# Kernel tuning notes

Hardware: AMD Instinct MI355X
Metric: run time of the kernel (lower is better)

The kernel has to match this reference:

```python
import jax, jax.numpy as jnp
import numpy as np

B, C, O, H, W = 16, 256, 256, 64, 64
T_DIM, E, K = 512, 4, 3


def setup_inputs() -> dict:
    key = jax.random.key(0)
    ks = jax.random.split(key, 12)
    def rn(k, shape, s=0.02):
        return jax.random.normal(k, shape, jnp.float32) * s
    return dict(
        x=jax.random.normal(ks[0], (B, C, H, W), jnp.float32),
        time_emb=jax.random.normal(ks[1], (B, T_DIM), jnp.float32),
        Wq=rn(ks[2], (C, T_DIM)), bq=jnp.zeros((C,), jnp.float32),
        Wk=rn(ks[3], (C, C)), bk=jnp.zeros((C,), jnp.float32),
        Wv=rn(ks[4], (C, C)), bv=jnp.zeros((C,), jnp.float32),
        Wm1=rn(ks[5], (C // 4, C)), bm1=jnp.zeros((C // 4,), jnp.float32),
        Wm2=rn(ks[6], (C, C // 4)), bm2=jnp.zeros((C,), jnp.float32),
        Wc=rn(ks[7], (E, C)), bc=jnp.zeros((E,), jnp.float32),
        expert_w=rn(ks[8], (E, O, C, K, K), s=0.05),  # [E, O, C_in/groups, K, K]
        expert_b=rn(ks[9], (E, O), s=0.05),
    )


def reference(x, time_emb, Wq, bq, Wk, bk, Wv, bv, Wm1, bm1, Wm2, bm2, Wc, bc, expert_w, expert_b):
    # --- router (eval mode: no gating noise) ---
    pooled = x.mean(axis=(2, 3))                      # [B, C] == avg_pool over full HxW
    q = time_emb @ Wq.T + bq                          # [B, C]
    k = pooled @ Wk.T + bk                            # [B, C]
    attn = jax.nn.sigmoid(q * k)
    v = pooled @ Wv.T + bv
    x_att = v * attn
    h = jax.nn.gelu(x_att @ Wm1.T + bm1, approximate=False) @ Wm2.T + bm2
    x_mix = x_att + h
    logits = x_mix @ Wc.T + bc                        # [B, E]
    rw = jnp.tanh(logits)                             # routing weights [B, E]

    # --- per-sample expert-weight mixing ---
    w_eff = jnp.einsum('be,eoihw->boihw', rw, expert_w)  # [B, O, C, K, K]
    b_eff = rw @ expert_b                                 # [B, O]

    # --- per-sample conv (equivalent to groups=B trick) ---
    def conv_one(xb, wb):
        # xb: [C, H, W], wb: [O, C, K, K]
        return jax.lax.conv_general_dilated(
            xb[None], wb, window_strides=(1, 1), padding=[(1, 1), (1, 1)],
            dimension_numbers=('NCHW', 'OIHW', 'NCHW'))[0]

    out = jax.vmap(conv_one)(x, w_eff)                 # [B, O, H, W]
    return out + b_eff[:, :, None, None]
```

## Files before the change

### kernel.cpp

```cpp
#include <hip/hip_runtime.h>


typedef __bf16 bf16x8 __attribute__((ext_vector_type(8)));
typedef float f32x4 __attribute__((ext_vector_type(4)));

__device__ __forceinline__ unsigned short f2bf(float f) {
  union { float f; unsigned int u; } v;
  v.f = f;
  unsigned int r = v.u + 0x7FFFu + ((v.u >> 16) & 1u);
  return (unsigned short)(r >> 16);
}

__device__ __forceinline__ void load_lds16(const void* g, void* l) {
  __builtin_amdgcn_global_load_lds(
      (__attribute__((address_space(1))) void*)(void*)g,
      (__attribute__((address_space(3))) void*)l, 16, 0, 0);
}

__global__ void pool_kernel(const float* __restrict__ x, float* __restrict__ pooled) {
  int bc = blockIdx.x;
  const float* p = x + (size_t)bc * 4096;
  int t = threadIdx.x;
  float s = 0.f;
  for (int i = t; i < 4096; i += 256) s += p[i];
  __shared__ float red[4];
  #pragma unroll
  for (int off = 32; off > 0; off >>= 1) s += __shfl_down(s, off);
  if ((t & 63) == 0) red[t >> 6] = s;
  __syncthreads();
  if (t == 0) pooled[bc] = (red[0] + red[1] + red[2] + red[3]) * (1.0f / 4096.0f);
}

__global__ void transpose_kernel(const float* __restrict__ x, unsigned short* __restrict__ xT) {
  int bh = blockIdx.x;
  int b = bh >> 6, h = bh & 63;
  __shared__ unsigned short lds[256][68];
  int t = threadIdx.x;
  int w = t & 63, cg = t >> 6;
  for (int it = 0; it < 64; ++it) {
    int c = it * 4 + cg;
    float v = x[(((size_t)(b * 256 + c)) * 64 + h) * 64 + w];
    lds[c][w] = f2bf(v);
  }
  __syncthreads();
  size_t obase = (size_t)bh * 64 * 256;
  for (int ww = 0; ww < 64; ++ww) {
    xT[obase + (size_t)ww * 256 + t] = lds[t][ww];
  }
}

__global__ void router_kernel(
    const float* __restrict__ time_emb, const float* __restrict__ pooled,
    const float* __restrict__ Wq, const float* __restrict__ bq,
    const float* __restrict__ Wk, const float* __restrict__ bk,
    const float* __restrict__ Wv, const float* __restrict__ bv,
    const float* __restrict__ Wm1, const float* __restrict__ bm1,
    const float* __restrict__ Wm2, const float* __restrict__ bm2,
    const float* __restrict__ Wc, const float* __restrict__ bc,
    const float* __restrict__ expert_b,
    float* __restrict__ rw_out, float* __restrict__ beff_out) {
  int b = blockIdx.x, t = threadIdx.x;
  __shared__ float te[512], pl[256], xa[256], m1s[64], xms[256], rws[4];
  te[t] = time_emb[b * 512 + t];
  te[t + 256] = time_emb[b * 512 + 256 + t];
  pl[t] = pooled[b * 256 + t];
  __syncthreads();
  float q = bq[t], k = bk[t], v = bv[t];
  const float* wq = Wq + (size_t)t * 512;
  for (int i = 0; i < 512; ++i) q += te[i] * wq[i];
  const float* wk = Wk + (size_t)t * 256;
  const float* wv = Wv + (size_t)t * 256;
  for (int i = 0; i < 256; ++i) { float p = pl[i]; k += p * wk[i]; v += p * wv[i]; }
  float attn = 1.0f / (1.0f + expf(-(q * k)));
  float xatt = v * attn;
  xa[t] = xatt;
  __syncthreads();
  if (t < 64) {
    float s = bm1[t];
    const float* w1 = Wm1 + (size_t)t * 256;
    for (int i = 0; i < 256; ++i) s += xa[i] * w1[i];
    m1s[t] = 0.5f * s * (1.0f + erff(s * 0.7071067811865476f));
  }
  __syncthreads();
  float hsum = bm2[t];
  const float* w2 = Wm2 + (size_t)t * 64;
  for (int j = 0; j < 64; ++j) hsum += m1s[j] * w2[j];
  float xm = xatt + hsum;
  xms[t] = xm;
  __syncthreads();
  if (t < 4) {
    float s = bc[t];
    const float* wc = Wc + (size_t)t * 256;
    for (int i = 0; i < 256; ++i) s += xms[i] * wc[i];
    float r = tanhf(s);
    rws[t] = r;
    rw_out[b * 4 + t] = r;
  }
  __syncthreads();
  float be = 0.f;
  #pragma unroll
  for (int e = 0; e < 4; ++e) be += rws[e] * expert_b[e * 256 + t];
  beff_out[b * 256 + t] = be;
}

__global__ void wmix_kernel(const float* __restrict__ ew, const float* __restrict__ rw,
                            unsigned short* __restrict__ wmix) {
  int o = blockIdx.x & 255;
  int b0 = (blockIdx.x >> 8) << 2;
  int c = threadIdx.x;
  float wv[4][9];
  #pragma unroll
  for (int e = 0; e < 4; ++e) {
    const float* s = ew + (((size_t)e * 256 + o) * 256 + c) * 9;
    #pragma unroll
    for (int tt = 0; tt < 9; ++tt) wv[e][tt] = s[tt];
  }
  for (int b = b0; b < b0 + 4; ++b) {
    float r0 = rw[b * 4 + 0], r1 = rw[b * 4 + 1], r2 = rw[b * 4 + 2], r3 = rw[b * 4 + 3];
    #pragma unroll
    for (int tt = 0; tt < 9; ++tt) {
      float m = r0 * wv[0][tt] + r1 * wv[1][tt] + r2 * wv[2][tt] + r3 * wv[3][tt];
      wmix[(((size_t)(b * 256 + o)) * 9 + tt) * 256 + c] = f2bf(m);
    }
  }
}

__global__ __launch_bounds__(256, 2) void conv_kernel(
    const unsigned short* __restrict__ xT, const unsigned short* __restrict__ wmix,
    const float* __restrict__ beff, float* __restrict__ out) {
  __shared__ unsigned short As[128 * 32];
  __shared__ unsigned short Bs[4 * 66 * 32];
  int bid = blockIdx.x;
  int b = bid >> 6;
  int rem = bid & 63;
  int o0 = (rem >> 5) << 7;
  int h0 = (rem & 31) << 1;
  int tid = threadIdx.x;
  int wid = tid >> 6, lane = tid & 63;
  int lm = lane & 15, lg = lane >> 4;
  int wm = wid >> 1, wn = wid & 1;

  if (tid < 128) {
    int rr = tid >> 5, colw = ((tid >> 4) & 1) ? 65 : 0, cp = tid & 15;
    *(unsigned int*)&Bs[(rr * 66 + colw) * 32 + cp * 2] = 0u;
  }

  f32x4 acc[4][4];
  #pragma unroll
  for (int mf = 0; mf < 4; ++mf)
    #pragma unroll
    for (int nf = 0; nf < 4; ++nf)
      acc[mf][nf] = (f32x4){0.f, 0.f, 0.f, 0.f};

  int aoff[4];
  #pragma unroll
  for (int mf = 0; mf < 4; ++mf)
    aoff[mf] = (wm * 64 + mf * 16 + lm) * 32 + lg * 8;
  int bbase[4];
  #pragma unroll
  for (int nf = 0; nf < 4; ++nf) {
    int p = wn * 64 + nf * 16 + lm;
    int hr = p >> 6, w = p & 63;
    bbase[nf] = (hr * 66 + w) * 32 + lg * 8;
  }

  const unsigned short* xTb = xT + (size_t)b * 4096 * 256;
  const unsigned short* wmb = wmix + ((size_t)b * 256 + o0) * 9 * 256;

  for (int cc = 0; cc < 8; ++cc) {
    int c0 = cc * 32;
    {
      int r = wid;
      int hh = h0 - 1 + r;
      unsigned short* dst = &Bs[(r * 66 + 1) * 32];
      if (hh >= 0 && hh < 64) {
        const unsigned short* src = xTb + (size_t)hh * 64 * 256 + c0;
        #pragma unroll
        for (int qq = 0; qq < 4; ++qq) {
          int wq = qq * 16 + (lane >> 2);
          int slot = lane & 3;
          load_lds16(src + (size_t)wq * 256 + slot * 8, dst + qq * 512);
        }
      } else {
        #pragma unroll
        for (int qq = 0; qq < 4; ++qq) {
          *(uint4*)&dst[qq * 512 + lane * 8] = make_uint4(0u, 0u, 0u, 0u);
        }
      }
    }
    #pragma unroll
    for (int tap = 0; tap < 9; ++tap) {
      {
        const unsigned short* asrc = wmb + (size_t)tap * 256 + c0;
        #pragma unroll
        for (int qq = 0; qq < 2; ++qq) {
          int row = wid * 32 + qq * 16 + (lane >> 2);
          int slot = lane & 3;
          load_lds16(asrc + (size_t)row * (9 * 256) + slot * 8,
                     &As[(wid * 32 + qq * 16) * 32]);
        }
      }
      __syncthreads();
      int kh = tap / 3, kw = tap % 3;
      int tshift = (kh * 66 + kw) * 32;
      bf16x8 af[4], bfr[4];
      #pragma unroll
      for (int mf = 0; mf < 4; ++mf) af[mf] = *(const bf16x8*)&As[aoff[mf]];
      #pragma unroll
      for (int nf = 0; nf < 4; ++nf) bfr[nf] = *(const bf16x8*)&Bs[bbase[nf] + tshift];
      #pragma unroll
      for (int mf = 0; mf < 4; ++mf)
        #pragma unroll
        for (int nf = 0; nf < 4; ++nf)
          acc[mf][nf] = __builtin_amdgcn_mfma_f32_16x16x32_bf16(af[mf], bfr[nf], acc[mf][nf], 0, 0, 0);
      __syncthreads();
    }
  }

  float be[4][4];
  #pragma unroll
  for (int mf = 0; mf < 4; ++mf)
    #pragma unroll
    for (int r = 0; r < 4; ++r)
      be[mf][r] = beff[b * 256 + o0 + wm * 64 + mf * 16 + lg * 4 + r];
  #pragma unroll
  for (int mf = 0; mf < 4; ++mf) {
    int o = o0 + wm * 64 + mf * 16 + lg * 4;
    #pragma unroll
    for (int nf = 0; nf < 4; ++nf) {
      int p = wn * 64 + nf * 16 + lm;
      int h = h0 + (p >> 6), w = p & 63;
      float* op = out + (((size_t)(b * 256 + o)) * 64 + h) * 64 + w;
      #pragma unroll
      for (int r = 0; r < 4; ++r) {
        op[(size_t)r * 4096] = acc[mf][nf][r] + be[mf][r];
      }
    }
  }
}

extern "C" void kernel_launch(void* const* d_in, const int* in_sizes, int n_in,
                              void* d_out, int out_size, void* d_ws, size_t ws_size,
                              hipStream_t stream) {
  const float* x        = (const float*)d_in[0];
  const float* time_emb = (const float*)d_in[1];
  const float* Wq = (const float*)d_in[2];
  const float* bq = (const float*)d_in[3];
  const float* Wk = (const float*)d_in[4];
  const float* bk = (const float*)d_in[5];
  const float* Wv = (const float*)d_in[6];
  const float* bv = (const float*)d_in[7];
  const float* Wm1 = (const float*)d_in[8];
  const float* bm1 = (const float*)d_in[9];
  const float* Wm2 = (const float*)d_in[10];
  const float* bm2 = (const float*)d_in[11];
  const float* Wc = (const float*)d_in[12];
  const float* bc = (const float*)d_in[13];
  const float* expert_w = (const float*)d_in[14];
  const float* expert_b = (const float*)d_in[15];
  float* out = (float*)d_out;

  char* ws = (char*)d_ws;
  float* pooled = (float*)(ws + 0);
  float* rw     = (float*)(ws + 16384);
  float* beff   = (float*)(ws + 16384 + 1024);
  unsigned short* xT   = (unsigned short*)(ws + 65536);
  unsigned short* wmix = (unsigned short*)(ws + 65536 + 33554432);

  pool_kernel<<<4096, 256, 0, stream>>>(x, pooled);
  transpose_kernel<<<1024, 256, 0, stream>>>(x, xT);
  router_kernel<<<16, 256, 0, stream>>>(time_emb, pooled, Wq, bq, Wk, bk, Wv, bv,
                                        Wm1, bm1, Wm2, bm2, Wc, bc, expert_b, rw, beff);
  wmix_kernel<<<1024, 256, 0, stream>>>(expert_w, rw, wmix);
  conv_kernel<<<1024, 256, 0, stream>>>(xT, wmix, beff, out);
}
```

Measured before the change: 166.2 us.

## Fuse pooling into transpose, re-layout operands, double-buffer conv LDS staging

Pooling now happens inside the transpose kernel, which writes per-row partial sums that the router reduces, so the separate pool pass over x goes away. Both xT and wmix move to channel-slice-major layouts (8 channels per 16-byte slot) so global-to-LDS loads are contiguous, and wmix handles 8 batches per block. The conv kernel double-buffers A and B tiles so the next tap's loads overlap the current MFMAs, which leaves one barrier per tap instead of two. It also raises occupancy to 3 blocks per SM and remaps block IDs across batches; this costs more LDS and register pressure.

```diff
diff --git a/kernel.cpp b/kernel.cpp
--- a/kernel.cpp
+++ b/kernel.cpp
@@ -1,8 +1,10 @@
 #include <hip/hip_runtime.h>
-
 
 typedef __bf16 bf16x8 __attribute__((ext_vector_type(8)));
 typedef float f32x4 __attribute__((ext_vector_type(4)));
+
+#define APLANE 1040
+#define BPLANE 2128
 
 __device__ __forceinline__ unsigned short f2bf(float f) {
   union { float f; unsigned int u; } v;
@@ -17,40 +19,35 @@
       (__attribute__((address_space(3))) void*)l, 16, 0, 0);
 }
 
-__global__ void pool_kernel(const float* __restrict__ x, float* __restrict__ pooled) {
-  int bc = blockIdx.x;
-  const float* p = x + (size_t)bc * 4096;
-  int t = threadIdx.x;
-  float s = 0.f;
-  for (int i = t; i < 4096; i += 256) s += p[i];
-  __shared__ float red[4];
-  #pragma unroll
-  for (int off = 32; off > 0; off >>= 1) s += __shfl_down(s, off);
-  if ((t & 63) == 0) red[t >> 6] = s;
-  __syncthreads();
-  if (t == 0) pooled[bc] = (red[0] + red[1] + red[2] + red[3]) * (1.0f / 4096.0f);
-}
-
-__global__ void transpose_kernel(const float* __restrict__ x, unsigned short* __restrict__ xT) {
-  int bh = blockIdx.x;
-  int b = bh >> 6, h = bh & 63;
-  __shared__ unsigned short lds[256][68];
-  int t = threadIdx.x;
-  int w = t & 63, cg = t >> 6;
+__global__ void transpose_kernel(const float* __restrict__ x, unsigned short* __restrict__ xT,
+                                 float* __restrict__ part) {
+  int bh = blockIdx.x, b = bh >> 6, h = bh & 63;
+  __shared__ unsigned short lds[64 * 264];
+  __shared__ float psum[256];
+  int t = threadIdx.x, lane = t & 63, wv = t >> 6;
+  const float* xb = x + (size_t)b * 1048576 + h * 64;
   for (int it = 0; it < 64; ++it) {
-    int c = it * 4 + cg;
-    float v = x[(((size_t)(b * 256 + c)) * 64 + h) * 64 + w];
-    lds[c][w] = f2bf(v);
-  }
-  __syncthreads();
-  size_t obase = (size_t)bh * 64 * 256;
-  for (int ww = 0; ww < 64; ++ww) {
-    xT[obase + (size_t)ww * 256 + t] = lds[t][ww];
-  }
+    int c = it * 4 + wv;
+    float v = xb[(size_t)c * 4096 + lane];
+    lds[lane * 264 + c] = f2bf(v);
+    float s = v;
+    #pragma unroll
+    for (int off = 32; off; off >>= 1) s += __shfl_xor(s, off);
+    if (lane == 0) psum[c] = s;
+  }
+  __syncthreads();
+  size_t ob = (size_t)bh * 16384;
+  #pragma unroll
+  for (int it = 0; it < 8; ++it) {
+    int sl = it * 4 + wv;
+    uint4 u = *(const uint4*)&lds[lane * 264 + sl * 8];
+    *(uint4*)&xT[ob + ((size_t)sl * 64 + lane) * 8] = u;
+  }
+  if (t < 256) part[(size_t)bh * 256 + t] = psum[t];
 }
 
 __global__ void router_kernel(
-    const float* __restrict__ time_emb, const float* __restrict__ pooled,
+    const float* __restrict__ time_emb, const float* __restrict__ part,
     const float* __restrict__ Wq, const float* __restrict__ bq,
     const float* __restrict__ Wk, const float* __restrict__ bk,
     const float* __restrict__ Wv, const float* __restrict__ bv,
@@ -63,7 +60,12 @@
   __shared__ float te[512], pl[256], xa[256], m1s[64], xms[256], rws[4];
   te[t] = time_emb[b * 512 + t];
   te[t + 256] = time_emb[b * 512 + 256 + t];
-  pl[t] = pooled[b * 256 + t];
+  {
+    float s = 0.f;
+    const float* pp = part + (size_t)b * 16384 + t;
+    for (int hh = 0; hh < 64; ++hh) s += pp[hh * 256];
+    pl[t] = s * (1.0f / 4096.0f);
+  }
   __syncthreads();
   float q = bq[t], k = bk[t], v = bv[t];
   const float* wq = Wq + (size_t)t * 512;
@@ -106,8 +108,11 @@
 __global__ void wmix_kernel(const float* __restrict__ ew, const float* __restrict__ rw,
                             unsigned short* __restrict__ wmix) {
   int o = blockIdx.x & 255;
-  int b0 = (blockIdx.x >> 8) << 2;
+  int bh = blockIdx.x >> 8;
   int c = threadIdx.x;
+  __shared__ float rsh[64];
+  if (c < 64) rsh[c] = rw[c];
+  __syncthreads();
   float wv[4][9];
   #pragma unroll
   for (int e = 0; e < 4; ++e) {
@@ -115,24 +120,25 @@
     #pragma unroll
     for (int tt = 0; tt < 9; ++tt) wv[e][tt] = s[tt];
   }
-  for (int b = b0; b < b0 + 4; ++b) {
-    float r0 = rw[b * 4 + 0], r1 = rw[b * 4 + 1], r2 = rw[b * 4 + 2], r3 = rw[b * 4 + 3];
+  int sl = c >> 3, cj = c & 7;
+  for (int b = bh * 8; b < bh * 8 + 8; ++b) {
+    float r0 = rsh[b * 4], r1 = rsh[b * 4 + 1], r2 = rsh[b * 4 + 2], r3 = rsh[b * 4 + 3];
     #pragma unroll
     for (int tt = 0; tt < 9; ++tt) {
       float m = r0 * wv[0][tt] + r1 * wv[1][tt] + r2 * wv[2][tt] + r3 * wv[3][tt];
-      wmix[(((size_t)(b * 256 + o)) * 9 + tt) * 256 + c] = f2bf(m);
-    }
-  }
-}
-
-__global__ __launch_bounds__(256, 2) void conv_kernel(
+      wmix[(((size_t)(b * 9 + tt) * 32 + sl) * 256 + o) * 8 + cj] = f2bf(m);
+    }
+  }
+}
+
+__global__ __launch_bounds__(256, 3) void conv_kernel(
     const unsigned short* __restrict__ xT, const unsigned short* __restrict__ wmix,
     const float* __restrict__ beff, float* __restrict__ out) {
-  __shared__ unsigned short As[128 * 32];
-  __shared__ unsigned short Bs[4 * 66 * 32];
+  __shared__ unsigned short As[2][4 * APLANE];
+  __shared__ unsigned short Bs[2][4 * BPLANE];
   int bid = blockIdx.x;
-  int b = bid >> 6;
-  int rem = bid & 63;
+  int b = ((bid & 7) << 1) | ((bid >> 9) & 1);
+  int rem = (bid >> 3) & 63;
   int o0 = (rem >> 5) << 7;
   int h0 = (rem & 31) << 1;
   int tid = threadIdx.x;
@@ -140,9 +146,35 @@
   int lm = lane & 15, lg = lane >> 4;
   int wm = wid >> 1, wn = wid & 1;
 
-  if (tid < 128) {
-    int rr = tid >> 5, colw = ((tid >> 4) & 1) ? 65 : 0, cp = tid & 15;
-    *(unsigned int*)&Bs[(rr * 66 + colw) * 32 + cp * 2] = 0u;
+  const unsigned short* xTb = xT + (size_t)b * 64 * 16384;
+  const unsigned short* wmixb = wmix + (size_t)b * 9 * 32 * 2048;
+
+  auto stageA = [&](int buf, int tap, int cc) {
+    const unsigned short* src =
+        wmixb + ((size_t)(tap * 32 + cc * 4 + wid) * 256 + o0) * 8 + lane * 8;
+    unsigned short* dst = &As[buf][wid * APLANE];
+    load_lds16(src, dst);
+    load_lds16(src + 512, dst + 512);
+  };
+  auto stageB = [&](int buf, int cc) {
+    int hh = h0 - 1 + wid;
+    unsigned short* dstp = &Bs[buf][(wid * 66 + 1) * 8];
+    if (hh >= 0 && hh < 64) {
+      const unsigned short* src = xTb + (size_t)hh * 16384 + cc * 2048 + lane * 8;
+      #pragma unroll
+      for (int q = 0; q < 4; ++q)
+        load_lds16(src + q * 512, dstp + q * BPLANE);
+    } else {
+      uint4 z = make_uint4(0u, 0u, 0u, 0u);
+      #pragma unroll
+      for (int q = 0; q < 4; ++q)
+        *(uint4*)&dstp[q * BPLANE + lane * 8] = z;
+    }
+  };
+
+  if (tid < 64) {
+    int bufi = tid >> 5, sl = (tid >> 3) & 3, hh = (tid >> 1) & 3, cl = (tid & 1) ? 65 : 0;
+    *(uint4*)&Bs[bufi][sl * BPLANE + (hh * 66 + cl) * 8] = make_uint4(0u, 0u, 0u, 0u);
   }
 
   f32x4 acc[4][4];
@@ -152,69 +184,45 @@
     for (int nf = 0; nf < 4; ++nf)
       acc[mf][nf] = (f32x4){0.f, 0.f, 0.f, 0.f};
 
-  int aoff[4];
+  int aoff[4], boff[4];
   #pragma unroll
   for (int mf = 0; mf < 4; ++mf)
-    aoff[mf] = (wm * 64 + mf * 16 + lm) * 32 + lg * 8;
-  int bbase[4];
-  #pragma unroll
-  for (int nf = 0; nf < 4; ++nf) {
-    int p = wn * 64 + nf * 16 + lm;
-    int hr = p >> 6, w = p & 63;
-    bbase[nf] = (hr * 66 + w) * 32 + lg * 8;
-  }
-
-  const unsigned short* xTb = xT + (size_t)b * 4096 * 256;
-  const unsigned short* wmb = wmix + ((size_t)b * 256 + o0) * 9 * 256;
-
+    aoff[mf] = lg * APLANE + (wm * 64 + mf * 16 + lm) * 8;
+  #pragma unroll
+  for (int nf = 0; nf < 4; ++nf)
+    boff[nf] = lg * BPLANE + (wn * 66 + nf * 16 + lm) * 8;
+
+  stageB(0, 0);
+  stageA(0, 0, 0);
+  __syncthreads();
+
+  int abuf = 0, bbuf = 0;
   for (int cc = 0; cc < 8; ++cc) {
-    int c0 = cc * 32;
-    {
-      int r = wid;
-      int hh = h0 - 1 + r;
-      unsigned short* dst = &Bs[(r * 66 + 1) * 32];
-      if (hh >= 0 && hh < 64) {
-        const unsigned short* src = xTb + (size_t)hh * 64 * 256 + c0;
-        #pragma unroll
-        for (int qq = 0; qq < 4; ++qq) {
-          int wq = qq * 16 + (lane >> 2);
-          int slot = lane & 3;
-          load_lds16(src + (size_t)wq * 256 + slot * 8, dst + qq * 512);
-        }
-      } else {
-        #pragma unroll
-        for (int qq = 0; qq < 4; ++qq) {
-          *(uint4*)&dst[qq * 512 + lane * 8] = make_uint4(0u, 0u, 0u, 0u);
-        }
+    #pragma unroll
+    for (int tap = 0; tap < 9; ++tap) {
+      if (tap < 8) {
+        stageA(abuf ^ 1, tap + 1, cc);
+      } else if (cc < 7) {
+        stageA(abuf ^ 1, 0, cc + 1);
+        stageB(bbuf ^ 1, cc + 1);
       }
-    }
-    #pragma unroll
-    for (int tap = 0; tap < 9; ++tap) {
-      {
-        const unsigned short* asrc = wmb + (size_t)tap * 256 + c0;
-        #pragma unroll
-        for (int qq = 0; qq < 2; ++qq) {
-          int row = wid * 32 + qq * 16 + (lane >> 2);
-          int slot = lane & 3;
-          load_lds16(asrc + (size_t)row * (9 * 256) + slot * 8,
-                     &As[(wid * 32 + qq * 16) * 32]);
-        }
-      }
-      __syncthreads();
-      int kh = tap / 3, kw = tap % 3;
-      int tshift = (kh * 66 + kw) * 32;
+      const int kh = tap / 3, kw = tap % 3;
       bf16x8 af[4], bfr[4];
       #pragma unroll
-      for (int mf = 0; mf < 4; ++mf) af[mf] = *(const bf16x8*)&As[aoff[mf]];
-      #pragma unroll
-      for (int nf = 0; nf < 4; ++nf) bfr[nf] = *(const bf16x8*)&Bs[bbase[nf] + tshift];
+      for (int mf = 0; mf < 4; ++mf)
+        af[mf] = *(const bf16x8*)&As[abuf][aoff[mf]];
+      #pragma unroll
+      for (int nf = 0; nf < 4; ++nf)
+        bfr[nf] = *(const bf16x8*)&Bs[bbuf][boff[nf] + (kh * 66 + kw) * 8];
       #pragma unroll
       for (int mf = 0; mf < 4; ++mf)
         #pragma unroll
         for (int nf = 0; nf < 4; ++nf)
           acc[mf][nf] = __builtin_amdgcn_mfma_f32_16x16x32_bf16(af[mf], bfr[nf], acc[mf][nf], 0, 0, 0);
       __syncthreads();
-    }
+      abuf ^= 1;
+    }
+    bbuf ^= 1;
   }
 
   float be[4][4];
@@ -232,9 +240,8 @@
       int h = h0 + (p >> 6), w = p & 63;
       float* op = out + (((size_t)(b * 256 + o)) * 64 + h) * 64 + w;
       #pragma unroll
-      for (int r = 0; r < 4; ++r) {
+      for (int r = 0; r < 4; ++r)
         op[(size_t)r * 4096] = acc[mf][nf][r] + be[mf][r];
-      }
     }
   }
 }
@@ -261,16 +268,15 @@
   float* out = (float*)d_out;
 
   char* ws = (char*)d_ws;
-  float* pooled = (float*)(ws + 0);
-  float* rw     = (float*)(ws + 16384);
-  float* beff   = (float*)(ws + 16384 + 1024);
-  unsigned short* xT   = (unsigned short*)(ws + 65536);
-  unsigned short* wmix = (unsigned short*)(ws + 65536 + 33554432);
-
-  pool_kernel<<<4096, 256, 0, stream>>>(x, pooled);
-  transpose_kernel<<<1024, 256, 0, stream>>>(x, xT);
-  router_kernel<<<16, 256, 0, stream>>>(time_emb, pooled, Wq, bq, Wk, bk, Wv, bv,
+  float* rw   = (float*)(ws + 0);
+  float* beff = (float*)(ws + 1024);
+  float* part = (float*)(ws + 20480);
+  unsigned short* xT   = (unsigned short*)(ws + 1069056);
+  unsigned short* wmix = (unsigned short*)(ws + 1069056 + 33554432);
+
+  transpose_kernel<<<1024, 256, 0, stream>>>(x, xT, part);
+  router_kernel<<<16, 256, 0, stream>>>(time_emb, part, Wq, bq, Wk, bk, Wv, bv,
                                         Wm1, bm1, Wm2, bm2, Wc, bc, expert_b, rw, beff);
-  wmix_kernel<<<1024, 256, 0, stream>>>(expert_w, rw, wmix);
+  wmix_kernel<<<512, 256, 0, stream>>>(expert_w, rw, wmix);
   conv_kernel<<<1024, 256, 0, stream>>>(xT, wmix, beff, out);
 }
```

Measured after the change: 192.5 us. 15.9% more time.
